# Kernel tuning notes

Hardware: AMD Instinct MI355X
Metric: run time of the kernel (lower is better)

## Reference

```python
import jax, jax.numpy as jnp
import numpy as np
from jax import lax

EPS = 1e-5  # BatchNorm eps (torch default)


def _bn_relu_conv3x3_s2(x, bn_w, bn_b, bn_m, bn_v, w, b):
    # eval-mode BatchNorm2d -> ReLU -> conv3x3 stride 2 pad 1 (NCHW)
    inv = bn_w / jnp.sqrt(bn_v + EPS)
    y = x * inv[None, :, None, None] + (bn_b - bn_m * inv)[None, :, None, None]
    y = jax.nn.relu(y)
    y = lax.conv_general_dilated(y, w, window_strides=(2, 2),
                                 padding=((1, 1), (1, 1)),
                                 dimension_numbers=("NCHW", "OIHW", "NCHW"))
    return y + b[None, :, None, None]


def _avgpool2x2(x):
    B, C, H, W = x.shape
    return x.reshape(B, C, H // 2, 2, W // 2, 2).mean(axis=(3, 5))


def setup_inputs() -> dict:
    key = jax.random.key(0)
    ks = jax.random.split(key, 24)
    C, C3 = 128, 128 // 3
    d = {"x": jax.random.normal(ks[0], (8, C, 96, 96), jnp.float32)}
    for i, p in enumerate(["f", "g", "h"]):
        base = 1 + i * 6
        d[p + "_bn_w"] = jax.random.uniform(ks[base], (C,), jnp.float32, 0.5, 1.5)
        d[p + "_bn_b"] = jax.random.normal(ks[base + 1], (C,), jnp.float32) * 0.1
        d[p + "_bn_m"] = jax.random.normal(ks[base + 2], (C,), jnp.float32) * 0.1
        d[p + "_bn_v"] = jax.random.uniform(ks[base + 3], (C,), jnp.float32, 0.5, 1.5)
        d[p + "_w"] = jax.random.normal(ks[base + 4], (C, C, 3, 3), jnp.float32) * (1.0 / np.sqrt(9 * C))
        d[p + "_b"] = jax.random.normal(ks[base + 5], (C,), jnp.float32) * 0.01
    d["se_cw"] = jax.random.normal(ks[19], (C3, 2 * C), jnp.float32) * (1.0 / np.sqrt(2 * C))
    d["se_cb"] = jax.random.normal(ks[20], (C3,), jnp.float32) * 0.01
    d["se_uw"] = jax.random.normal(ks[21], (C, C3), jnp.float32) * (1.0 / np.sqrt(C3))
    d["se_ub"] = jax.random.normal(ks[22], (C,), jnp.float32) * 0.01
    d["gamma"] = jax.random.normal(ks[23], (1,), jnp.float32) * 0.5
    return d


def reference(x, f_bn_w, f_bn_b, f_bn_m, f_bn_v, f_w, f_b,
              g_bn_w, g_bn_b, g_bn_m, g_bn_v, g_w, g_b,
              h_bn_w, h_bn_b, h_bn_m, h_bn_v, h_w, h_b,
              se_cw, se_cb, se_uw, se_ub, gamma):
    B, C, H, W = x.shape
    left = _avgpool2x2(x)  # isPrimary=False branch -> [B,C,H/2,W/2]

    f = _bn_relu_conv3x3_s2(x, f_bn_w, f_bn_b, f_bn_m, f_bn_v, f_w, f_b)
    g = _bn_relu_conv3x3_s2(x, g_bn_w, g_bn_b, g_bn_m, g_bn_v, g_w, g_b)
    h = _bn_relu_conv3x3_s2(x, h_bn_w, h_bn_b, h_bn_m, h_bn_v, h_w, h_b)

    Ho, Wo = f.shape[2], f.shape[3]
    N = Ho * Wo
    ff = f.reshape(B, C, N)
    gg = g.reshape(B, C, N)
    hh = h.reshape(B, C, N)

    # s = softmax over last axis of f^T g : [B, N, N]
    scores = jnp.einsum("bcn,bcm->bnm", ff, gg)
    attn = jax.nn.softmax(scores, axis=2)
    s = jnp.einsum("bcn,bnm->bcm", hh, attn).reshape(B, C, Ho, Wo)
    s = gamma[0] * s

    # CompetitiveSE: global-avg x and s -> concat(2C) -> ReLU/1x1(C//3) -> ReLU/1x1(C)
    wx = x.mean(axis=(2, 3))          # [B, C]
    ws = s.mean(axis=(2, 3))          # [B, C]
    wcat = jnp.concatenate([wx, ws], axis=1)  # [B, 2C]
    se = jax.nn.relu(wcat) @ se_cw.T + se_cb
    se = jax.nn.relu(se) @ se_uw.T + se_ub    # [B, C]

    return (left + s) * (1.0 + se[:, :, None, None])
```

## Files before the change

kernel.cpp:

```cpp
#include <hip/hip_runtime.h>
#include <hip/hip_bf16.h>

#define B_   8
#define C_   128
#define H_   96
#define W_   96
#define HP_  98
#define HO_  48
#define N_   2304
#define K_CONV 1152
#define PLANE_IN  9216
#define TOT_OUT (B_*C_*N_)

typedef __attribute__((ext_vector_type(8))) short          s16x8;
typedef __attribute__((ext_vector_type(8))) unsigned short u16x8;
typedef __attribute__((ext_vector_type(4))) unsigned short u16x4;
typedef __attribute__((ext_vector_type(4))) float          f32x4;

#define SW(row, q)   (((row) << 6) + ((((q) ^ (((row) >> 1) & 3))) << 4))
#define SW8(row, q)  (((row) << 7) + ((((q) ^ ((row) & 7))) << 4))
#define SW16(row, q) (((row) << 8) + ((((q) ^ ((row) & 15))) << 4))

__device__ __forceinline__ ushort f2bf(float f) {
  __hip_bfloat16 h = __float2bfloat16(f);
  return *reinterpret_cast<ushort*>(&h);
}

__device__ __forceinline__ float block_reduce_sum_256(float v) {
  #pragma unroll
  for (int o = 32; o > 0; o >>= 1) v += __shfl_down(v, o, 64);
  __shared__ float r[4];
  int lane = threadIdx.x & 63, wv = threadIdx.x >> 6;
  if (lane == 0) r[wv] = v;
  __syncthreads();
  float s = 0.f;
  if (threadIdx.x == 0) s = r[0] + r[1] + r[2] + r[3];
  __syncthreads();
  return s;
}

__global__ void k_prep(const float* __restrict__ w0, const float* __restrict__ b0,
                       const float* __restrict__ m0, const float* __restrict__ v0,
                       const float* __restrict__ w1, const float* __restrict__ b1,
                       const float* __restrict__ m1, const float* __restrict__ v1,
                       const float* __restrict__ w2, const float* __restrict__ b2,
                       const float* __restrict__ m2, const float* __restrict__ v2,
                       float* __restrict__ inv, float* __restrict__ beta) {
  int p = blockIdx.x, c = threadIdx.x;
  const float* w = (p == 0 ? w0 : p == 1 ? w1 : w2);
  const float* bb = (p == 0 ? b0 : p == 1 ? b1 : b2);
  const float* m = (p == 0 ? m0 : p == 1 ? m1 : m2);
  const float* v = (p == 0 ? v0 : p == 1 ? v1 : v2);
  if (c < C_) {
    float iv = w[c] / sqrtf(v[c] + 1e-5f);
    inv[p * 128 + c] = iv;
    beta[p * 128 + c] = bb[c] - m[c] * iv;
  }
}

__global__ __launch_bounds__(256) void k_prep_w(const float* __restrict__ w0,
                                                const float* __restrict__ w1,
                                                const float* __restrict__ w2,
                                                ushort* __restrict__ o0,
                                                ushort* __restrict__ o1,
                                                ushort* __restrict__ o2) {
  int p = blockIdx.y;
  const float* w = (p == 0 ? w0 : p == 1 ? w1 : w2);
  ushort* wb = (p == 0 ? o0 : p == 1 ? o1 : o2);
  int id = blockIdx.x * 256 + threadIdx.x;
  if (id >= C_ * K_CONV) return;
  int co = id / K_CONV, rem = id - co * K_CONV;
  int tap = rem >> 7, ci = rem & 127;
  wb[id] = f2bf(w[co * K_CONV + ci * 9 + tap]);
}

__global__ __launch_bounds__(256) void k_prep_y(const float* __restrict__ x,
                                                const float* __restrict__ pinv,
                                                const float* __restrict__ pbeta,
                                                ushort* __restrict__ y0,
                                                ushort* __restrict__ y1,
                                                ushort* __restrict__ y2) {
  const int h1 = blockIdx.x, b = blockIdx.y, t = threadIdx.x;
  ushort* ys[3] = {y0 + (size_t)b * HP_ * HP_ * C_,
                   y1 + (size_t)b * HP_ * HP_ * C_,
                   y2 + (size_t)b * HP_ * HP_ * C_};
  u16x8 zer = (u16x8)0;
  if (h1 == 0 || h1 == HP_ - 1) {
    for (int p = 0; p < 3; ++p)
      for (int g = t; g < HP_ * C_ / 8; g += 256)
        *(u16x8*)(ys[p] + (size_t)h1 * HP_ * C_ + g * 8) = zer;
    return;
  }
  __shared__ float xs[128][97];
  const int h = h1 - 1;
  const float* xb = x + (size_t)b * C_ * PLANE_IN + h * W_;
  for (int id = t; id < 128 * 24; id += 256) {
    int ci = id / 24, w4 = id - ci * 24;
    float4 v = *(const float4*)(xb + (size_t)ci * PLANE_IN + w4 * 4);
    xs[ci][w4 * 4 + 0] = v.x; xs[ci][w4 * 4 + 1] = v.y;
    xs[ci][w4 * 4 + 2] = v.z; xs[ci][w4 * 4 + 3] = v.w;
  }
  __syncthreads();
  if (t < 32) {
    int side = t >> 4, cg = t & 15;
    for (int p = 0; p < 3; ++p)
      *(u16x8*)(ys[p] + ((size_t)h1 * HP_ + (side ? HP_ - 1 : 0)) * C_ + cg * 8) = zer;
  }
  for (int p = 0; p < 3; ++p) {
    const float* inv = pinv + p * 128;
    const float* bet = pbeta + p * 128;
    for (int g = t; g < 96 * 16; g += 256) {
      int wdx = g >> 4, cg = g & 15;
      u16x8 o;
      #pragma unroll
      for (int k = 0; k < 8; ++k) {
        int ci = cg * 8 + k;
        o[k] = f2bf(fmaxf(xs[ci][wdx] * inv[ci] + bet[ci], 0.f));
      }
      *(u16x8*)(ys[p] + ((size_t)h1 * HP_ + (wdx + 1)) * C_ + cg * 8) = o;
    }
  }
}

__global__ __launch_bounds__(256) void k_meanx(const float* __restrict__ x,
                                               float* __restrict__ wcat) {
  int bc = blockIdx.x;
  const float* p = x + (size_t)bc * PLANE_IN;
  float s = 0.f;
  for (int i = threadIdx.x; i < PLANE_IN; i += 256) s += p[i];
  s = block_reduce_sum_256(s);
  if (threadIdx.x == 0) {
    int b = bc >> 7, c = bc & 127;
    wcat[b * 256 + c] = fmaxf(s * (1.f / PLANE_IN), 0.f);
  }
}

__global__ __launch_bounds__(256) void k_conv3(
    const ushort* __restrict__ y0, const ushort* __restrict__ y1, const ushort* __restrict__ y2,
    const ushort* __restrict__ w0, const ushort* __restrict__ w1, const ushort* __restrict__ w2,
    const float* __restrict__ bi0, const float* __restrict__ bi1, const float* __restrict__ bi2,
    ushort* __restrict__ fo, ushort* __restrict__ go, ushort* __restrict__ ho) {
  __shared__ __align__(16) char smem[16384];
  char* As = smem;
  char* Bs = smem + 8192;
  const int br = blockIdx.y, b = blockIdx.z, n0 = blockIdx.x * 64;
  const int t = threadIdx.x, l = t & 63, w = t >> 6;
  const ushort* yb = (br == 0 ? y0 : br == 1 ? y1 : y2) + (size_t)b * HP_ * HP_ * C_;
  const ushort* wb = (br == 0 ? w0 : br == 1 ? w1 : w2);
  const float* bias = (br == 0 ? bi0 : br == 1 ? bi1 : bi2);
  const int pos = t >> 2, q = t & 3;
  const int n_glob = n0 + pos;
  const int oh = n_glob / HO_, ow = n_glob - oh * HO_;
  const int mh = (w & 1) * 64, nh = (w >> 1) * 32;
  f32x4 acc[4][2];
  #pragma unroll
  for (int i = 0; i < 4; ++i)
    #pragma unroll
    for (int j = 0; j < 2; ++j) acc[i][j] = (f32x4)0.f;

  for (int k0 = 0; k0 < K_CONV; k0 += 32) {
    int tap = k0 >> 7, ci0 = k0 & 127;
    int kh = tap / 3, kw = tap - kh * 3;
    #pragma unroll
    for (int g2 = 0; g2 < 2; ++g2) {
      int g = t + g2 * 256, row = g >> 2, qq = g & 3;
      u16x8 d = *(const u16x8*)(wb + row * K_CONV + k0 + qq * 8);
      *(u16x8*)(As + SW(row, qq)) = d;
    }
    {
      int h1 = 2 * oh + kh, w1 = 2 * ow + kw;
      u16x8 d = *(const u16x8*)(yb + ((size_t)h1 * HP_ + w1) * C_ + ci0 + q * 8);
      *(u16x8*)(Bs + SW(pos, q)) = d;
    }
    __syncthreads();
    s16x8 af[4], bf[2];
    #pragma unroll
    for (int i = 0; i < 4; ++i) {
      int r = mh + i * 16 + (l & 15);
      af[i] = *(const s16x8*)(As + SW(r, (l >> 4)));
    }
    #pragma unroll
    for (int j = 0; j < 2; ++j) {
      int r = nh + j * 16 + (l & 15);
      bf[j] = *(const s16x8*)(Bs + SW(r, (l >> 4)));
    }
    #pragma unroll
    for (int i = 0; i < 4; ++i)
      #pragma unroll
      for (int j = 0; j < 2; ++j)
        acc[i][j] = __builtin_amdgcn_mfma_f32_16x16x32_bf16(af[i], bf[j], acc[i][j], 0, 0, 0);
    __syncthreads();
  }

  if (br < 2) {
    ushort* out = (br == 0) ? fo : go;
    ushort* tb = (ushort*)smem;
    #pragma unroll
    for (int i = 0; i < 4; ++i) {
      int co4 = mh + i * 16 + (l >> 4) * 4;
      float4 bi = *(const float4*)&bias[co4];
      float bia[4] = {bi.x, bi.y, bi.z, bi.w};
      #pragma unroll
      for (int j = 0; j < 2; ++j) {
        int pp = nh + j * 16 + (l & 15);
        #pragma unroll
        for (int r = 0; r < 4; ++r)
          tb[pp * 128 + co4 + r] = f2bf(acc[i][j][r] + bia[r]);
      }
    }
    __syncthreads();
    #pragma unroll
    for (int it = 0; it < 4; ++it) {
      int g = t + it * 256;
      int row = g >> 4, gg = g & 15;
      u16x8 d = *(const u16x8*)(tb + row * 128 + gg * 8);
      *(u16x8*)(out + ((size_t)b * N_ + n0 + row) * C_ + gg * 8) = d;
    }
  } else {
    ushort* tb = (ushort*)smem;
    #pragma unroll
    for (int i = 0; i < 4; ++i) {
      int co4 = mh + i * 16 + (l >> 4) * 4;
      float4 bi = *(const float4*)&bias[co4];
      float bia[4] = {bi.x, bi.y, bi.z, bi.w};
      #pragma unroll
      for (int j = 0; j < 2; ++j) {
        int pp = nh + j * 16 + (l & 15);
        #pragma unroll
        for (int r = 0; r < 4; ++r)
          tb[(co4 + r) * 64 + pp] = f2bf(acc[i][j][r] + bia[r]);
      }
    }
    __syncthreads();
    for (int g = t; g < 1024; g += 256) {
      int co = g >> 3, off2 = (g & 7) * 8;
      u16x8 d = *(const u16x8*)(tb + co * 64 + off2);
      *(u16x8*)(ho + ((size_t)b * C_ + co) * N_ + n0 + off2) = d;
    }
  }
}

__global__ __launch_bounds__(256) void k_stats(const ushort* __restrict__ f,
                                               const ushort* __restrict__ g,
                                               float2* __restrict__ pstats) {
  __shared__ __align__(16) char smem[32768];
  const int blk = blockIdx.x;
  const int b = blk & 7, t2 = blk >> 3;
  const int n0 = (t2 % 36) * 64, mz = t2 / 36;
  const int t = threadIdx.x, l = t & 63, w = t >> 6, lo = l & 15, quad = l >> 4;
  const ushort* fb = f + (size_t)b * N_ * C_;
  const ushort* gb = g + (size_t)b * N_ * C_;
  s16x8 af[4];
  #pragma unroll
  for (int ks = 0; ks < 4; ++ks)
    af[ks] = *(const s16x8*)(fb + (size_t)(n0 + w * 16 + lo) * C_ + (ks * 4 + quad) * 8);
  float mloc[4], lloc[4];
  #pragma unroll
  for (int r = 0; r < 4; ++r) { mloc[r] = -1e30f; lloc[r] = 0.f; }
  const int m_beg = mz * 576;

  for (int i9 = 0; i9 < 9; ++i9) {
    char* gs = smem + ((i9 & 1) << 14);
    int m0 = m_beg + i9 * 64;
    #pragma unroll
    for (int it = 0; it < 4; ++it) {
      int G = t + it * 256, row = G >> 4, g16 = G & 15;
      *(u16x8*)(gs + SW16(row, g16)) = *(const u16x8*)(gb + (size_t)(m0 + row) * C_ + g16 * 8);
    }
    __syncthreads();
    f32x4 acc[4];
    #pragma unroll
    for (int j = 0; j < 4; ++j) acc[j] = (f32x4)0.f;
    __builtin_amdgcn_s_setprio(1);
    #pragma unroll
    for (int ks = 0; ks < 4; ++ks)
      #pragma unroll
      for (int j = 0; j < 4; ++j) {
        s16x8 bf = *(const s16x8*)(gs + SW16(j * 16 + lo, ks * 4 + quad));
        acc[j] = __builtin_amdgcn_mfma_f32_16x16x32_bf16(af[ks], bf, acc[j], 0, 0, 0);
      }
    __builtin_amdgcn_s_setprio(0);
    #pragma unroll
    for (int r = 0; r < 4; ++r) {
      float vmax = fmaxf(fmaxf(acc[0][r], acc[1][r]), fmaxf(acc[2][r], acc[3][r]));
      float mn = fmaxf(mloc[r], vmax);
      lloc[r] = lloc[r] * __expf(mloc[r] - mn) +
                __expf(acc[0][r] - mn) + __expf(acc[1][r] - mn) +
                __expf(acc[2][r] - mn) + __expf(acc[3][r] - mn);
      mloc[r] = mn;
    }
  }
  #pragma unroll
  for (int r = 0; r < 4; ++r) {
    #pragma unroll
    for (int o = 1; o < 16; o <<= 1) {
      float mo = __shfl_xor(mloc[r], o, 64);
      float lo2 = __shfl_xor(lloc[r], o, 64);
      float mn = fmaxf(mloc[r], mo);
      lloc[r] = lloc[r] * __expf(mloc[r] - mn) + lo2 * __expf(mo - mn);
      mloc[r] = mn;
    }
  }
  if (lo == 0) {
    #pragma unroll
    for (int r = 0; r < 4; ++r)
      pstats[((size_t)mz * B_ + b) * N_ + n0 + w * 16 + quad * 4 + r] =
          make_float2(mloc[r], lloc[r]);
  }
}

__global__ __launch_bounds__(256) void k_stats_red(const float2* __restrict__ p,
                                                   float2* __restrict__ stats) {
  int idx = blockIdx.x * 256 + threadIdx.x;
  if (idx >= B_ * N_) return;
  float mx = -1e30f, ls = 0.f;
  #pragma unroll
  for (int z = 0; z < 4; ++z) {
    float2 s = p[(size_t)z * B_ * N_ + idx];
    float mn = fmaxf(mx, s.x);
    ls = ls * __expf(mx - mn) + s.y * __expf(s.x - mn);
    mx = mn;
  }
  stats[idx] = make_float2(mx, ls);
}

__global__ __launch_bounds__(256) void k_attn_out(const ushort* __restrict__ f,
                                                  const ushort* __restrict__ g,
                                                  const ushort* __restrict__ h,
                                                  const float2* __restrict__ stats,
                                                  float* __restrict__ spart) {
  __shared__ __align__(16) char smem[35072];
  char* gs = smem;
  char* pTb = smem + 16384;
  const int blk = blockIdx.x;
  const int b = blk & 7, t2 = blk >> 3;
  const int m0 = (t2 % 36) * 64, nz = t2 / 36;
  const int t = threadIdx.x, l = t & 63, w = t >> 6, lo = l & 15, quad = l >> 4;
  const ushort* fb = f + (size_t)b * N_ * C_;
  const ushort* gb = g + (size_t)b * N_ * C_;
  const ushort* hb = h + (size_t)b * C_ * N_;
  const float2* stb = stats + (size_t)b * N_;
  #pragma unroll
  for (int it = 0; it < 4; ++it) {
    int G = t + it * 256, row = G >> 4, g16 = G & 15;
    *(u16x8*)(gs + SW16(row, g16)) = *(const u16x8*)(gb + (size_t)(m0 + row) * C_ + g16 * 8);
  }
  __syncthreads();
  f32x4 accs[2][4];
  #pragma unroll
  for (int i = 0; i < 2; ++i)
    #pragma unroll
    for (int j = 0; j < 4; ++j) accs[i][j] = (f32x4)0.f;
  const int n_beg = nz * 576;

  for (int i9 = 0; i9 < 9; ++i9) {
    int nb = n_beg + i9 * 64;
    char* pT = pTb + ((i9 & 1) << 13);
    s16x8 af[4], ah[2][2];
    #pragma unroll
    for (int ks = 0; ks < 4; ++ks)
      af[ks] = *(const s16x8*)(fb + (size_t)(nb + w * 16 + lo) * C_ + (ks * 4 + quad) * 8);
    #pragma unroll
    for (int i = 0; i < 2; ++i)
      #pragma unroll
      for (int ks = 0; ks < 2; ++ks)
        ah[i][ks] = *(const s16x8*)(hb + (size_t)((2 * w + i) * 16 + lo) * N_ + nb + (ks * 4 + quad) * 8);
    float mxr[4], ilr[4];
    #pragma unroll
    for (int r = 0; r < 4; ++r) {
      float2 st = stb[nb + w * 16 + quad * 4 + r];
      mxr[r] = st.x; ilr[r] = 1.f / st.y;
    }
    f32x4 sc[4];
    #pragma unroll
    for (int j = 0; j < 4; ++j) sc[j] = (f32x4)0.f;
    __builtin_amdgcn_s_setprio(1);
    #pragma unroll
    for (int ks = 0; ks < 4; ++ks)
      #pragma unroll
      for (int j = 0; j < 4; ++j) {
        s16x8 bg = *(const s16x8*)(gs + SW16(j * 16 + lo, ks * 4 + quad));
        sc[j] = __builtin_amdgcn_mfma_f32_16x16x32_bf16(af[ks], bg, sc[j], 0, 0, 0);
      }
    __builtin_amdgcn_s_setprio(0);
    const int nl = w * 16 + quad * 4;
    #pragma unroll
    for (int j = 0; j < 4; ++j) {
      u16x4 pv;
      #pragma unroll
      for (int r = 0; r < 4; ++r)
        pv[r] = f2bf(__expf(sc[j][r] - mxr[r]) * ilr[r]);
      *(u16x4*)(pT + SW8(j * 16 + lo, nl >> 3) + (nl & 7) * 2) = pv;
    }
    __syncthreads();
    __builtin_amdgcn_s_setprio(1);
    #pragma unroll
    for (int ks = 0; ks < 2; ++ks)
      #pragma unroll
      for (int j = 0; j < 4; ++j) {
        s16x8 bp = *(const s16x8*)(pT + SW8(j * 16 + lo, ks * 4 + quad));
        accs[0][j] = __builtin_amdgcn_mfma_f32_16x16x32_bf16(ah[0][ks], bp, accs[0][j], 0, 0, 0);
        accs[1][j] = __builtin_amdgcn_mfma_f32_16x16x32_bf16(ah[1][ks], bp, accs[1][j], 0, 0, 0);
      }
    __builtin_amdgcn_s_setprio(0);
  }
  __syncthreads();
  float* ss = (float*)smem;
  #pragma unroll
  for (int i = 0; i < 2; ++i) {
    int c0 = (2 * w + i) * 16 + quad * 4;
    #pragma unroll
    for (int j = 0; j < 4; ++j) {
      int m = j * 16 + lo;
      #pragma unroll
      for (int r = 0; r < 4; ++r)
        ss[(c0 + r) * 68 + m] = accs[i][j][r];
    }
  }
  __syncthreads();
  float* outp = spart + (size_t)nz * TOT_OUT + (size_t)b * C_ * N_ + m0;
  #pragma unroll
  for (int it = 0; it < 8; ++it) {
    int idx = t + it * 256;
    int c = idx >> 4, mq = idx & 15;
    float4 v = *(const float4*)&ss[c * 68 + mq * 4];
    *(float4*)&outp[(size_t)c * N_ + mq * 4] = v;
  }
}

__global__ __launch_bounds__(256) void k_sred(const float* __restrict__ spart,
                                              const float* __restrict__ gammap,
                                              float* __restrict__ sbuf) {
  int idx = blockIdx.x * 256 + threadIdx.x;
  if (idx >= TOT_OUT) return;
  float s = spart[idx] + spart[(size_t)TOT_OUT + idx] +
            spart[2 * (size_t)TOT_OUT + idx] + spart[3 * (size_t)TOT_OUT + idx];
  sbuf[idx] = gammap[0] * s;
}

__global__ __launch_bounds__(256) void k_means(const float* __restrict__ s,
                                               float* __restrict__ wcat) {
  int bc = blockIdx.x;
  const float* p = s + (size_t)bc * N_;
  float sm = 0.f;
  for (int i = threadIdx.x; i < N_; i += 256) sm += p[i];
  sm = block_reduce_sum_256(sm);
  if (threadIdx.x == 0) {
    int b = bc >> 7, c = bc & 127;
    wcat[b * 256 + 128 + c] = fmaxf(sm * (1.f / N_), 0.f);
  }
}

__global__ __launch_bounds__(128) void k_se(const float* __restrict__ wcat,
                                            const float* __restrict__ cw,
                                            const float* __restrict__ cb,
                                            const float* __restrict__ uw,
                                            const float* __restrict__ ub,
                                            float* __restrict__ se) {
  const int b = blockIdx.x, t = threadIdx.x;
  __shared__ float wc[256];
  __shared__ float s1[42];
  wc[t] = wcat[b * 256 + t];
  wc[128 + t] = wcat[b * 256 + 128 + t];
  __syncthreads();
  if (t < 42) {
    float a = cb[t];
    const float* r = cw + (size_t)t * 256;
    for (int k = 0; k < 256; ++k) a += wc[k] * r[k];
    s1[t] = fmaxf(a, 0.f);
  }
  __syncthreads();
  {
    float a = ub[t];
    const float* r = uw + (size_t)t * 42;
    for (int j = 0; j < 42; ++j) a += s1[j] * r[j];
    se[b * 128 + t] = a;
  }
}

__global__ __launch_bounds__(256) void k_final(const float* __restrict__ x,
                                               const float* __restrict__ s,
                                               const float* __restrict__ se,
                                               float* __restrict__ out) {
  int idx = blockIdx.x * 256 + threadIdx.x;
  if (idx >= TOT_OUT) return;
  int m  = idx % N_;
  int bc = idx / N_;
  int oh = m / HO_, ow = m - oh * HO_;
  const float* xp = x + (size_t)bc * PLANE_IN;
  int ih = oh * 2, iw = ow * 2;
  float l = 0.25f * (xp[ih * W_ + iw] + xp[ih * W_ + iw + 1] +
                     xp[(ih + 1) * W_ + iw] + xp[(ih + 1) * W_ + iw + 1]);
  out[idx] = (l + s[idx]) * (1.f + se[bc]);
}

extern "C" void kernel_launch(void* const* d_in, const int* in_sizes, int n_in,
                              void* d_out, int out_size, void* d_ws, size_t ws_size,
                              hipStream_t stream) {
  (void)in_sizes; (void)n_in; (void)out_size; (void)ws_size;
  const float* x    = (const float*)d_in[0];
  const float* bnw[3] = {(const float*)d_in[1],  (const float*)d_in[7],  (const float*)d_in[13]};
  const float* bnb[3] = {(const float*)d_in[2],  (const float*)d_in[8],  (const float*)d_in[14]};
  const float* bnm[3] = {(const float*)d_in[3],  (const float*)d_in[9],  (const float*)d_in[15]};
  const float* bnv[3] = {(const float*)d_in[4],  (const float*)d_in[10], (const float*)d_in[16]};
  const float* cw_[3] = {(const float*)d_in[5],  (const float*)d_in[11], (const float*)d_in[17]};
  const float* cbb[3] = {(const float*)d_in[6],  (const float*)d_in[12], (const float*)d_in[18]};
  const float* secw = (const float*)d_in[19];
  const float* secb = (const float*)d_in[20];
  const float* seuw = (const float*)d_in[21];
  const float* seub = (const float*)d_in[22];
  const float* gamma = (const float*)d_in[23];
  float* out = (float*)d_out;

  char* ws = (char*)d_ws;
  size_t off = 0;
  auto alloc = [&](size_t bytes) -> char* {
    char* p = ws + off;
    off = (off + bytes + 255) & ~(size_t)255;
    return p;
  };
  ushort* yp[3];
  for (int p = 0; p < 3; ++p) yp[p] = (ushort*)alloc((size_t)B_ * HP_ * HP_ * C_ * 2);
  ushort* wb[3];
  for (int p = 0; p < 3; ++p) wb[p] = (ushort*)alloc((size_t)C_ * K_CONV * 2);
  ushort* fbuf = (ushort*)alloc((size_t)B_ * N_ * C_ * 2);
  ushort* gbuf = (ushort*)alloc((size_t)B_ * N_ * C_ * 2);
  ushort* hbuf = (ushort*)alloc((size_t)B_ * C_ * N_ * 2);
  float2* pstats = (float2*)alloc((size_t)4 * B_ * N_ * 8);
  float2* stats  = (float2*)alloc((size_t)B_ * N_ * 8);
  float*  spart = (float*)alloc((size_t)4 * TOT_OUT * 4);
  float*  sbuf = (float*)alloc((size_t)TOT_OUT * 4);
  float*  wcat = (float*)alloc(B_ * 256 * 4);
  float*  sebuf = (float*)alloc(B_ * 128 * 4);
  float*  pinv  = (float*)alloc(3 * 128 * 4);
  float*  pbeta = (float*)alloc(3 * 128 * 4);

  k_prep<<<3, 128, 0, stream>>>(bnw[0], bnb[0], bnm[0], bnv[0],
                                bnw[1], bnb[1], bnm[1], bnv[1],
                                bnw[2], bnb[2], bnm[2], bnv[2], pinv, pbeta);
  k_prep_w<<<dim3((C_ * K_CONV + 255) / 256, 3), 256, 0, stream>>>(
      cw_[0], cw_[1], cw_[2], wb[0], wb[1], wb[2]);
  k_prep_y<<<dim3(HP_, B_), 256, 0, stream>>>(x, pinv, pbeta, yp[0], yp[1], yp[2]);
  k_meanx<<<B_ * C_, 256, 0, stream>>>(x, wcat);

  k_conv3<<<dim3(N_ / 64, 3, B_), 256, 0, stream>>>(yp[0], yp[1], yp[2],
                                                    wb[0], wb[1], wb[2],
                                                    cbb[0], cbb[1], cbb[2],
                                                    fbuf, gbuf, hbuf);

  k_stats<<<1152, 256, 0, stream>>>(fbuf, gbuf, pstats);
  k_stats_red<<<(B_ * N_ + 255) / 256, 256, 0, stream>>>(pstats, stats);
  k_attn_out<<<1152, 256, 0, stream>>>(fbuf, gbuf, hbuf, stats, spart);
  k_sred<<<(TOT_OUT + 255) / 256, 256, 0, stream>>>(spart, gamma, sbuf);

  k_means<<<B_ * C_, 256, 0, stream>>>(sbuf, wcat);
  k_se<<<B_, 128, 0, stream>>>(wcat, secw, secb, seuw, seub, sebuf);

  k_final<<<(TOT_OUT + 255) / 256, 256, 0, stream>>>(x, sbuf, sebuf, out);
}
```

Measured before the change: 297.8 us.

## Software-pipeline G loads in stats kernel and Q/PV stages in attention kernel

```diff
diff --git a/kernel.cpp b/kernel.cpp
--- a/kernel.cpp
+++ b/kernel.cpp
@@ -259,15 +259,30 @@
   for (int r = 0; r < 4; ++r) { mloc[r] = -1e30f; lloc[r] = 0.f; }
   const int m_beg = mz * 576;
 
+  u16x8 st[4];
+  #pragma unroll
+  for (int it = 0; it < 4; ++it) {
+    int G = t + it * 256, row = G >> 4, g16 = G & 15;
+    st[it] = *(const u16x8*)(gb + (size_t)(m_beg + row) * C_ + g16 * 8);
+  }
+  #pragma unroll
+  for (int it = 0; it < 4; ++it) {
+    int G = t + it * 256, row = G >> 4, g16 = G & 15;
+    *(u16x8*)(smem + SW16(row, g16)) = st[it];
+  }
+  __syncthreads();
+
+  #pragma unroll
   for (int i9 = 0; i9 < 9; ++i9) {
     char* gs = smem + ((i9 & 1) << 14);
-    int m0 = m_beg + i9 * 64;
-    #pragma unroll
-    for (int it = 0; it < 4; ++it) {
-      int G = t + it * 256, row = G >> 4, g16 = G & 15;
-      *(u16x8*)(gs + SW16(row, g16)) = *(const u16x8*)(gb + (size_t)(m0 + row) * C_ + g16 * 8);
-    }
-    __syncthreads();
+    if (i9 < 8) {
+      int m0n = m_beg + (i9 + 1) * 64;
+      #pragma unroll
+      for (int it = 0; it < 4; ++it) {
+        int G = t + it * 256, row = G >> 4, g16 = G & 15;
+        st[it] = *(const u16x8*)(gb + (size_t)(m0n + row) * C_ + g16 * 8);
+      }
+    }
     f32x4 acc[4];
     #pragma unroll
     for (int j = 0; j < 4; ++j) acc[j] = (f32x4)0.f;
@@ -289,6 +304,15 @@
                 __expf(acc[2][r] - mn) + __expf(acc[3][r] - mn);
       mloc[r] = mn;
     }
+    if (i9 < 8) {
+      char* gn = smem + (((i9 + 1) & 1) << 14);
+      #pragma unroll
+      for (int it = 0; it < 4; ++it) {
+        int G = t + it * 256, row = G >> 4, g16 = G & 15;
+        *(u16x8*)(gn + SW16(row, g16)) = st[it];
+      }
+    }
+    __syncthreads();
   }
   #pragma unroll
   for (int r = 0; r < 4; ++r) {
@@ -310,7 +334,7 @@
 }
 
 __global__ __launch_bounds__(256) void k_stats_red(const float2* __restrict__ p,
-                                                   float2* __restrict__ stats) {
+                                                   float* __restrict__ astat) {
   int idx = blockIdx.x * 256 + threadIdx.x;
   if (idx >= B_ * N_) return;
   float mx = -1e30f, ls = 0.f;
@@ -321,13 +345,13 @@
     ls = ls * __expf(mx - mn) + s.y * __expf(s.x - mn);
     mx = mn;
   }
-  stats[idx] = make_float2(mx, ls);
+  astat[idx] = -mx - __logf(ls);
 }
 
 __global__ __launch_bounds__(256) void k_attn_out(const ushort* __restrict__ f,
                                                   const ushort* __restrict__ g,
                                                   const ushort* __restrict__ h,
-                                                  const float2* __restrict__ stats,
+                                                  const float* __restrict__ astat,
                                                   float* __restrict__ spart) {
   __shared__ __align__(16) char smem[35072];
   char* gs = smem;
@@ -339,13 +363,12 @@
   const ushort* fb = f + (size_t)b * N_ * C_;
   const ushort* gb = g + (size_t)b * N_ * C_;
   const ushort* hb = h + (size_t)b * C_ * N_;
-  const float2* stb = stats + (size_t)b * N_;
+  const float* ab = astat + (size_t)b * N_;
   #pragma unroll
   for (int it = 0; it < 4; ++it) {
     int G = t + it * 256, row = G >> 4, g16 = G & 15;
     *(u16x8*)(gs + SW16(row, g16)) = *(const u16x8*)(gb + (size_t)(m0 + row) * C_ + g16 * 8);
   }
-  __syncthreads();
   f32x4 accs[2][4];
   #pragma unroll
   for (int i = 0; i < 2; ++i)
@@ -353,24 +376,28 @@
     for (int j = 0; j < 4; ++j) accs[i][j] = (f32x4)0.f;
   const int n_beg = nz * 576;
 
-  for (int i9 = 0; i9 < 9; ++i9) {
-    int nb = n_beg + i9 * 64;
-    char* pT = pTb + ((i9 & 1) << 13);
-    s16x8 af[4], ah[2][2];
+  s16x8 af[2][4];
+  s16x8 ahc[2][2];
+  float ax[2][4];
+
+  auto LOAD_AF = [&](int i, int p) {
+    int nb = n_beg + i * 64;
     #pragma unroll
     for (int ks = 0; ks < 4; ++ks)
-      af[ks] = *(const s16x8*)(fb + (size_t)(nb + w * 16 + lo) * C_ + (ks * 4 + quad) * 8);
-    #pragma unroll
-    for (int i = 0; i < 2; ++i)
+      af[p][ks] = *(const s16x8*)(fb + (size_t)(nb + w * 16 + lo) * C_ + (ks * 4 + quad) * 8);
+    float4 av = *(const float4*)(ab + nb + w * 16 + quad * 4);
+    ax[p][0] = av.x; ax[p][1] = av.y; ax[p][2] = av.z; ax[p][3] = av.w;
+  };
+  auto LOAD_AH = [&](int i) {
+    int nb = n_beg + i * 64;
+    #pragma unroll
+    for (int ii = 0; ii < 2; ++ii)
       #pragma unroll
       for (int ks = 0; ks < 2; ++ks)
-        ah[i][ks] = *(const s16x8*)(hb + (size_t)((2 * w + i) * 16 + lo) * N_ + nb + (ks * 4 + quad) * 8);
-    float mxr[4], ilr[4];
-    #pragma unroll
-    for (int r = 0; r < 4; ++r) {
-      float2 st = stb[nb + w * 16 + quad * 4 + r];
-      mxr[r] = st.x; ilr[r] = 1.f / st.y;
-    }
+        ahc[ii][ks] = *(const s16x8*)(hb + (size_t)((2 * w + ii) * 16 + lo) * N_ + nb + (ks * 4 + quad) * 8);
+  };
+  auto QKEXP = [&](int p) {
+    char* pT = pTb + (p << 13);
     f32x4 sc[4];
     #pragma unroll
     for (int j = 0; j < 4; ++j) sc[j] = (f32x4)0.f;
@@ -380,7 +407,7 @@
       #pragma unroll
       for (int j = 0; j < 4; ++j) {
         s16x8 bg = *(const s16x8*)(gs + SW16(j * 16 + lo, ks * 4 + quad));
-        sc[j] = __builtin_amdgcn_mfma_f32_16x16x32_bf16(af[ks], bg, sc[j], 0, 0, 0);
+        sc[j] = __builtin_amdgcn_mfma_f32_16x16x32_bf16(af[p][ks], bg, sc[j], 0, 0, 0);
       }
     __builtin_amdgcn_s_setprio(0);
     const int nl = w * 16 + quad * 4;
@@ -389,20 +416,38 @@
       u16x4 pv;
       #pragma unroll
       for (int r = 0; r < 4; ++r)
-        pv[r] = f2bf(__expf(sc[j][r] - mxr[r]) * ilr[r]);
+        pv[r] = f2bf(__expf(sc[j][r] + ax[p][r]));
       *(u16x4*)(pT + SW8(j * 16 + lo, nl >> 3) + (nl & 7) * 2) = pv;
     }
-    __syncthreads();
+  };
+  auto PV = [&](int p) {
+    char* pT = pTb + (p << 13);
     __builtin_amdgcn_s_setprio(1);
     #pragma unroll
     for (int ks = 0; ks < 2; ++ks)
       #pragma unroll
       for (int j = 0; j < 4; ++j) {
         s16x8 bp = *(const s16x8*)(pT + SW8(j * 16 + lo, ks * 4 + quad));
-        accs[0][j] = __builtin_amdgcn_mfma_f32_16x16x32_bf16(ah[0][ks], bp, accs[0][j], 0, 0, 0);
-        accs[1][j] = __builtin_amdgcn_mfma_f32_16x16x32_bf16(ah[1][ks], bp, accs[1][j], 0, 0, 0);
+        accs[0][j] = __builtin_amdgcn_mfma_f32_16x16x32_bf16(ahc[0][ks], bp, accs[0][j], 0, 0, 0);
+        accs[1][j] = __builtin_amdgcn_mfma_f32_16x16x32_bf16(ahc[1][ks], bp, accs[1][j], 0, 0, 0);
       }
     __builtin_amdgcn_s_setprio(0);
+  };
+
+  LOAD_AF(0, 0);
+  LOAD_AH(0);
+  __syncthreads();
+  QKEXP(0);
+  LOAD_AF(1, 1);
+  #pragma unroll
+  for (int i9 = 0; i9 < 9; ++i9) {
+    __syncthreads();
+    PV(i9 & 1);
+    if (i9 < 8) {
+      LOAD_AH(i9 + 1);
+      QKEXP((i9 + 1) & 1);
+      if (i9 < 7) LOAD_AF(i9 + 2, i9 & 1);
+    }
   }
   __syncthreads();
   float* ss = (float*)smem;
@@ -527,7 +572,7 @@
   ushort* gbuf = (ushort*)alloc((size_t)B_ * N_ * C_ * 2);
   ushort* hbuf = (ushort*)alloc((size_t)B_ * C_ * N_ * 2);
   float2* pstats = (float2*)alloc((size_t)4 * B_ * N_ * 8);
-  float2* stats  = (float2*)alloc((size_t)B_ * N_ * 8);
+  float*  astat  = (float*)alloc((size_t)B_ * N_ * 4);
   float*  spart = (float*)alloc((size_t)4 * TOT_OUT * 4);
   float*  sbuf = (float*)alloc((size_t)TOT_OUT * 4);
   float*  wcat = (float*)alloc(B_ * 256 * 4);
@@ -549,8 +594,8 @@
                                                     fbuf, gbuf, hbuf);
 
   k_stats<<<1152, 256, 0, stream>>>(fbuf, gbuf, pstats);
-  k_stats_red<<<(B_ * N_ + 255) / 256, 256, 0, stream>>>(pstats, stats);
-  k_attn_out<<<1152, 256, 0, stream>>>(fbuf, gbuf, hbuf, stats, spart);
+  k_stats_red<<<(B_ * N_ + 255) / 256, 256, 0, stream>>>(pstats, astat);
+  k_attn_out<<<1152, 256, 0, stream>>>(fbuf, gbuf, hbuf, astat, spart);
   k_sred<<<(TOT_OUT + 255) / 256, 256, 0, stream>>>(spart, gamma, sbuf);
 
   k_means<<<B_ * C_, 256, 0, stream>>>(sbuf, wcat);
```

New measurement: 292.2 us. About the same (-1.9%).
